# Kernel optimization log

Measured on AMD Instinct MI355X. Metric: run time of the kernel, lower is better.

The kernel has to match this reference:

```python
import jax, jax.numpy as jnp
import numpy as np

MARGIN = 1.0
SQUARED = False


def _pdist(v, squared):
    # pairwise Euclidean distances with zeroed diagonal, matching torch pdist()
    sq = jnp.sum(v * v, axis=1)
    d2 = jax.nn.relu(-2.0 * (v @ v.T) + sq[None, :] + sq[:, None])
    err = (d2 <= 0).astype(v.dtype)
    d = d2 if squared else jnp.sqrt(d2 + err * 1e-16)
    d = d * (1.0 - err)
    n = v.shape[0]
    return d * (1.0 - jnp.eye(n, dtype=v.dtype))


def setup_inputs() -> dict:
    key = jax.random.key(0)
    k1, k2 = jax.random.split(key)
    embeddings = jax.random.normal(k1, (384, 512), dtype=jnp.float32)
    labels = jax.random.randint(k2, (384,), 0, 64)
    return {"embeddings": embeddings, "labels": labels}


def reference(embeddings, labels):
    B = embeddings.shape[0]
    d = _pdist(embeddings, SQUARED)                      # [B,B]
    adj = labels[:, None] == labels[None, :]             # [B,B] same-label
    adj_not = ~adj
    # tiled mask: mask3[i,j,k] = adj_not[j,k] & (d[j,k] > d[j,i])
    # (i indexes the tile/repeat axis, j the pdist row, k the candidate negative)
    mask3 = (adj_not[None, :, :] & (d[None, :, :] > d.T[:, :, None])).astype(d.dtype)
    mask_final = (jnp.sum(mask3, axis=2) > 0).T          # [B,B], [i,j]: exists neg outside
    # masked_min over k (torch masked_min): subtract row max, min of masked diff, add back
    row_max = jnp.max(d, axis=1)                         # [B]
    neg_out = jnp.min((d[None, :, :] - row_max[None, :, None]) * mask3, axis=2) + row_max[None, :]
    neg_out = neg_out.T                                  # [i,j]: min d[i,k] with adj_not & d[i,k] > d[i,j]
    # masked_max over k (torch masked_max) for negatives_inside
    row_min = jnp.min(d, axis=1)                         # [B]
    neg_in = jnp.max((d - row_min[:, None]) * adj_not.astype(d.dtype), axis=1) + row_min  # [B]
    neg_in = jnp.broadcast_to(neg_in[:, None], (B, B))
    semihard = jnp.where(mask_final, neg_out, neg_in)
    loss_mat = d - semihard + MARGIN
    mask_pos = adj.astype(d.dtype) - jnp.eye(B, dtype=d.dtype)
    num_pos = jnp.sum(mask_pos)
    return jnp.sum(jax.nn.relu(loss_mat * mask_pos)) / num_pos
```

## Files before the change

kernel.cpp:

```cpp
#include <hip/hip_runtime.h>

#define NB 384
#define ND 512
#define FLT_BIG 3.0e38f


__global__ __launch_bounds__(64) void prep_kernel(const float* __restrict__ V,
                                                  const int* __restrict__ labels,
                                                  float* __restrict__ sq,
                                                  float* __restrict__ npos) {
  const int bx = blockIdx.x;
  const int lane = threadIdx.x;
  if (bx < NB) {
    const float4* row = (const float4*)(V + (size_t)bx * ND);
    float4 v0 = row[lane * 2];
    float4 v1 = row[lane * 2 + 1];
    float acc = v0.x * v0.x + v0.y * v0.y + v0.z * v0.z + v0.w * v0.w +
                v1.x * v1.x + v1.y * v1.y + v1.z * v1.z + v1.w * v1.w;
#pragma unroll
    for (int off = 32; off; off >>= 1) acc += __shfl_xor(acc, off);
    if (lane == 0) sq[bx] = acc;
  } else {
    __shared__ int cnt[64];
    cnt[lane] = 0;
    __syncthreads();
#pragma unroll
    for (int i = 0; i < 6; ++i) atomicAdd(&cnt[labels[lane + 64 * i]], 1);
    __syncthreads();
    int c = cnt[lane];
    int s = c * c;
#pragma unroll
    for (int off = 32; off; off >>= 1) s += __shfl_xor(s, off);
    if (lane == 0) npos[0] = (float)(s - NB);
  }
}

__global__ __launch_bounds__(256) void gram_kernel(const float* __restrict__ V,
                                                   float* __restrict__ G) {
  __shared__ float As[64][68];
  __shared__ float Bs[64][68];
  const int tid = threadIdx.x;
  const int a0 = blockIdx.y * 64, b0 = blockIdx.x * 64, k0 = blockIdx.z * 64;

#pragma unroll
  for (int it = 0; it < 4; ++it) {
    int f = tid + it * 256;
    int row = f >> 4, c4 = (f & 15) << 2;
    *(float4*)&As[row][c4] = *(const float4*)&V[(size_t)(a0 + row) * ND + k0 + c4];
    *(float4*)&Bs[row][c4] = *(const float4*)&V[(size_t)(b0 + row) * ND + k0 + c4];
  }
  __syncthreads();

  const int tx = tid & 15, ty = tid >> 4;
  float acc[4][4] = {};
#pragma unroll
  for (int kk = 0; kk < 64; kk += 4) {
    float4 av[4], bv[4];
#pragma unroll
    for (int i = 0; i < 4; ++i) {
      av[i] = *(const float4*)&As[ty + 16 * i][kk];
      bv[i] = *(const float4*)&Bs[tx + 16 * i][kk];
    }
#pragma unroll
    for (int i = 0; i < 4; ++i)
#pragma unroll
      for (int j = 0; j < 4; ++j) {
        acc[i][j] = fmaf(av[i].x, bv[j].x, acc[i][j]);
        acc[i][j] = fmaf(av[i].y, bv[j].y, acc[i][j]);
        acc[i][j] = fmaf(av[i].z, bv[j].z, acc[i][j]);
        acc[i][j] = fmaf(av[i].w, bv[j].w, acc[i][j]);
      }
  }
#pragma unroll
  for (int i = 0; i < 4; ++i)
#pragma unroll
    for (int j = 0; j < 4; ++j)
      atomicAdd(&G[(size_t)(a0 + ty + 16 * i) * NB + (b0 + tx + 16 * j)], acc[i][j]);
}

__global__ __launch_bounds__(64) void loss_kernel(const float* __restrict__ G,
                                                  const float* __restrict__ sq,
                                                  const int* __restrict__ labels,
                                                  const float* __restrict__ npos,
                                                  float* __restrict__ out) {
  const int a = blockIdx.x;
  const int lane = threadIdx.x;
  const float sqa = sq[a];
  const int la = labels[a];

  float dk[6];
  int same[6];
  float neg_in = 0.0f;
#pragma unroll
  for (int i = 0; i < 6; ++i) {
    const int k = lane + (i << 6);
    const float g = G[(size_t)a * NB + k];
    float d2 = sqa + sq[k] - 2.0f * g;
    d2 = fmaxf(d2, 0.0f);
    float d = (d2 <= 0.0f) ? 0.0f : sqrtf(d2);
    if (k == a) d = 0.0f;
    dk[i] = d;
    same[i] = (labels[k] == la);
    if (!same[i]) neg_in = fmaxf(neg_in, d);
  }
#pragma unroll
  for (int off = 32; off; off >>= 1) neg_in = fmaxf(neg_in, __shfl_xor(neg_in, off));

  float rsum = 0.0f;
#pragma unroll 1
  for (int i = 0; i < 6; ++i) {
    const int k = lane + (i << 6);
    unsigned long long pm = __ballot(same[i] && (k != a));
    while (pm) {
      const int src = __builtin_ctzll(pm);
      pm &= pm - 1;
      const float db = __shfl(dk[i], src);
      float m = FLT_BIG;
#pragma unroll
      for (int t = 0; t < 6; ++t) {
        const float c = (!same[t] && dk[t] > db) ? dk[t] : FLT_BIG;
        m = fminf(m, c);
      }
#pragma unroll
      for (int off = 32; off; off >>= 1) m = fminf(m, __shfl_xor(m, off));
      const float semi = (m < 1.0e38f) ? m : neg_in;
      rsum += fmaxf(db - semi + 1.0f, 0.0f);
    }
  }
  if (lane == 0) atomicAdd(out, rsum / npos[0]);
}

extern "C" void kernel_launch(void* const* d_in, const int* in_sizes, int n_in,
                              void* d_out, int out_size, void* d_ws, size_t ws_size,
                              hipStream_t stream) {
  const float* V = (const float*)d_in[0];
  const int* labels = (const int*)d_in[1];
  float* outp = (float*)d_out;
  float* G = (float*)d_ws;
  float* sq = G + (size_t)NB * NB;
  float* npos = sq + NB;
  hipMemsetAsync(G, 0, (size_t)NB * NB * sizeof(float), stream);
  hipMemsetAsync(d_out, 0, sizeof(float), stream);
  prep_kernel<<<dim3(NB + 1), 64, 0, stream>>>(V, labels, sq, npos);
  gram_kernel<<<dim3(6, 6, 8), 256, 0, stream>>>(V, G);
  loss_kernel<<<dim3(NB), 64, 0, stream>>>(G, sq, labels, npos, outp);
}
```

Measured before the change: 75.90 us.

## Fuse prep into Gram kernel, exploit symmetry, replace atomics with split-K partials

```diff
diff --git a/kernel.cpp b/kernel.cpp
--- a/kernel.cpp
+++ b/kernel.cpp
@@ -2,83 +2,99 @@
 
 #define NB 384
 #define ND 512
+#define KS 8
 #define FLT_BIG 3.0e38f
 
 
-__global__ __launch_bounds__(64) void prep_kernel(const float* __restrict__ V,
-                                                  const int* __restrict__ labels,
-                                                  float* __restrict__ sq,
-                                                  float* __restrict__ npos) {
+__global__ __launch_bounds__(256) void gram_prep_kernel(const float* __restrict__ V,
+                                                        const int* __restrict__ labels,
+                                                        float* __restrict__ Gp,
+                                                        float* __restrict__ sq,
+                                                        float* __restrict__ npos,
+                                                        float* __restrict__ out0) {
   const int bx = blockIdx.x;
-  const int lane = threadIdx.x;
-  if (bx < NB) {
-    const float4* row = (const float4*)(V + (size_t)bx * ND);
-    float4 v0 = row[lane * 2];
-    float4 v1 = row[lane * 2 + 1];
-    float acc = v0.x * v0.x + v0.y * v0.y + v0.z * v0.z + v0.w * v0.w +
-                v1.x * v1.x + v1.y * v1.y + v1.z * v1.z + v1.w * v1.w;
-#pragma unroll
-    for (int off = 32; off; off >>= 1) acc += __shfl_xor(acc, off);
-    if (lane == 0) sq[bx] = acc;
-  } else {
-    __shared__ int cnt[64];
-    cnt[lane] = 0;
-    __syncthreads();
-#pragma unroll
-    for (int i = 0; i < 6; ++i) atomicAdd(&cnt[labels[lane + 64 * i]], 1);
-    __syncthreads();
-    int c = cnt[lane];
-    int s = c * c;
-#pragma unroll
-    for (int off = 32; off; off >>= 1) s += __shfl_xor(s, off);
-    if (lane == 0) npos[0] = (float)(s - NB);
-  }
-}
-
-__global__ __launch_bounds__(256) void gram_kernel(const float* __restrict__ V,
-                                                   float* __restrict__ G) {
-  __shared__ float As[64][68];
-  __shared__ float Bs[64][68];
   const int tid = threadIdx.x;
-  const int a0 = blockIdx.y * 64, b0 = blockIdx.x * 64, k0 = blockIdx.z * 64;
+  if (bx < 168) {
+    __shared__ float As[64][68];
+    __shared__ float Bs[64][68];
+    const int ks = bx / 21;
+    int rem = bx % 21;
+    int ti = 0, cnt = 6;
+    while (rem >= cnt) { rem -= cnt; --cnt; ++ti; }
+    const int tj = ti + rem;
+    const int a0 = ti * 64, b0 = tj * 64, k0 = ks * 64;
 
 #pragma unroll
-  for (int it = 0; it < 4; ++it) {
-    int f = tid + it * 256;
-    int row = f >> 4, c4 = (f & 15) << 2;
-    *(float4*)&As[row][c4] = *(const float4*)&V[(size_t)(a0 + row) * ND + k0 + c4];
-    *(float4*)&Bs[row][c4] = *(const float4*)&V[(size_t)(b0 + row) * ND + k0 + c4];
-  }
-  __syncthreads();
+    for (int it = 0; it < 4; ++it) {
+      int f = tid + it * 256;
+      int row = f >> 4, c4 = (f & 15) << 2;
+      *(float4*)&As[row][c4] = *(const float4*)&V[(size_t)(a0 + row) * ND + k0 + c4];
+      *(float4*)&Bs[row][c4] = *(const float4*)&V[(size_t)(b0 + row) * ND + k0 + c4];
+    }
+    __syncthreads();
 
-  const int tx = tid & 15, ty = tid >> 4;
-  float acc[4][4] = {};
+    const int tx = tid & 15, ty = tid >> 4;
+    float acc[4][4] = {};
 #pragma unroll
-  for (int kk = 0; kk < 64; kk += 4) {
-    float4 av[4], bv[4];
+    for (int kk = 0; kk < 64; kk += 4) {
+      float4 av[4], bv[4];
 #pragma unroll
-    for (int i = 0; i < 4; ++i) {
-      av[i] = *(const float4*)&As[ty + 16 * i][kk];
-      bv[i] = *(const float4*)&Bs[tx + 16 * i][kk];
+      for (int i = 0; i < 4; ++i) {
+        av[i] = *(const float4*)&As[ty + 16 * i][kk];
+        bv[i] = *(const float4*)&Bs[tx + 16 * i][kk];
+      }
+#pragma unroll
+      for (int i = 0; i < 4; ++i)
+#pragma unroll
+        for (int j = 0; j < 4; ++j) {
+          acc[i][j] = fmaf(av[i].x, bv[j].x, acc[i][j]);
+          acc[i][j] = fmaf(av[i].y, bv[j].y, acc[i][j]);
+          acc[i][j] = fmaf(av[i].z, bv[j].z, acc[i][j]);
+          acc[i][j] = fmaf(av[i].w, bv[j].w, acc[i][j]);
+        }
     }
+    float* Gk = Gp + (size_t)ks * NB * NB;
 #pragma unroll
     for (int i = 0; i < 4; ++i)
 #pragma unroll
       for (int j = 0; j < 4; ++j) {
-        acc[i][j] = fmaf(av[i].x, bv[j].x, acc[i][j]);
-        acc[i][j] = fmaf(av[i].y, bv[j].y, acc[i][j]);
-        acc[i][j] = fmaf(av[i].z, bv[j].z, acc[i][j]);
-        acc[i][j] = fmaf(av[i].w, bv[j].w, acc[i][j]);
+        const int ar = a0 + ty + 16 * i, bc = b0 + tx + 16 * j;
+        Gk[(size_t)ar * NB + bc] = acc[i][j];
+        Gk[(size_t)bc * NB + ar] = acc[i][j];
       }
+  } else if (bx < 174) {
+    const int r = (bx - 168) * 64 + (tid >> 2);
+    const int q = tid & 3;
+    const float4* p = (const float4*)(V + (size_t)r * ND + q * 128);
+    float s = 0.f;
+#pragma unroll 8
+    for (int i = 0; i < 32; ++i) {
+      float4 v = p[i];
+      s += v.x * v.x + v.y * v.y + v.z * v.z + v.w * v.w;
+    }
+    s += __shfl_xor(s, 1);
+    s += __shfl_xor(s, 2);
+    if (q == 0) sq[r] = s;
+  } else {
+    __shared__ int cnt[64];
+    if (tid < 64) cnt[tid] = 0;
+    __syncthreads();
+    for (int i = tid; i < NB; i += 256) atomicAdd(&cnt[labels[i]], 1);
+    __syncthreads();
+    if (tid < 64) {
+      int c = cnt[tid];
+      int s = c * c;
+#pragma unroll
+      for (int off = 32; off; off >>= 1) s += __shfl_xor(s, off);
+      if (tid == 0) {
+        npos[0] = (float)(s - NB);
+        out0[0] = 0.0f;
+      }
+    }
   }
-#pragma unroll
-  for (int i = 0; i < 4; ++i)
-#pragma unroll
-    for (int j = 0; j < 4; ++j)
-      atomicAdd(&G[(size_t)(a0 + ty + 16 * i) * NB + (b0 + tx + 16 * j)], acc[i][j]);
 }
 
-__global__ __launch_bounds__(64) void loss_kernel(const float* __restrict__ G,
+__global__ __launch_bounds__(64) void loss_kernel(const float* __restrict__ Gp,
                                                   const float* __restrict__ sq,
                                                   const int* __restrict__ labels,
                                                   const float* __restrict__ npos,
@@ -94,7 +110,9 @@
 #pragma unroll
   for (int i = 0; i < 6; ++i) {
     const int k = lane + (i << 6);
-    const float g = G[(size_t)a * NB + k];
+    float g = 0.f;
+#pragma unroll
+    for (int p = 0; p < KS; ++p) g += Gp[(size_t)p * NB * NB + (size_t)a * NB + k];
     float d2 = sqa + sq[k] - 2.0f * g;
     d2 = fmaxf(d2, 0.0f);
     float d = (d2 <= 0.0f) ? 0.0f : sqrtf(d2);
@@ -136,12 +154,9 @@
   const float* V = (const float*)d_in[0];
   const int* labels = (const int*)d_in[1];
   float* outp = (float*)d_out;
-  float* G = (float*)d_ws;
-  float* sq = G + (size_t)NB * NB;
+  float* Gp = (float*)d_ws;
+  float* sq = Gp + (size_t)KS * NB * NB;
   float* npos = sq + NB;
-  hipMemsetAsync(G, 0, (size_t)NB * NB * sizeof(float), stream);
-  hipMemsetAsync(d_out, 0, sizeof(float), stream);
-  prep_kernel<<<dim3(NB + 1), 64, 0, stream>>>(V, labels, sq, npos);
-  gram_kernel<<<dim3(6, 6, 8), 256, 0, stream>>>(V, G);
-  loss_kernel<<<dim3(NB), 64, 0, stream>>>(G, sq, labels, npos, outp);
+  gram_prep_kernel<<<dim3(175), 256, 0, stream>>>(V, labels, Gp, sq, npos, outp);
+  loss_kernel<<<dim3(NB), 64, 0, stream>>>(Gp, sq, labels, npos, outp);
 }
```

Result: faster. 69.47 us (-8.5%).
